# Kernel optimization log

Hardware: AMD Instinct MI355X
Metric: run time of the kernel (lower is better)

Reference implementation:

```python
import jax, jax.numpy as jnp
import numpy as np

EPS = 1.1920929e-07  # torch clamp_probs eps for float32
TEMP = 0.3           # sampler temperature T


def conv1d(x, w, b, pad):
    # x: [B, Cin, L], w: [Cout, Cin, K] -> [B, Cout, L']
    y = jax.lax.conv_general_dilated(x, w, window_strides=(1,), padding=[(pad, pad)],
                                     dimension_numbers=('NCH', 'OIH', 'NCH'))
    return y + b[None, :, None]


def setup_inputs() -> dict:
    key = jax.random.key(0)
    ks = jax.random.split(key, 20)
    B, L, V, E, F, H, K = 512, 512, 100000, 100, 100, 100, 10
    p = lambda i, shape: jax.random.normal(ks[i], shape, jnp.float32) * 0.02
    return {
        'x': jax.random.randint(ks[0], (B, L), 0, V, dtype=jnp.int32),
        'u': jax.random.uniform(ks[1], (B, K, L), dtype=jnp.float32),
        'emb': p(2, (V, E)),
        'conv1_w': p(3, (F, E, 3)), 'conv1_b': p(4, (F,)),
        'gi_w': p(5, (H, F)), 'gi_b': p(6, (H,)),
        'conv2_w': p(7, (H, F, 3)), 'conv2_b': p(8, (H,)),
        'li_w': p(9, (H, H, 3)), 'li_b': p(10, (H,)),
        'conv3_w': p(11, (F, 2 * H, 1)), 'conv3_b': p(12, (F,)),
        'conv4_w': p(13, (1, F, 1)), 'conv4_b': p(14, (1,)),
        'fc1_w': p(15, (H, E)), 'fc1_b': p(16, (H,)),
        'head_w': p(17, (1, H)), 'head_b': p(18, (1,)),
    }


def _ti_logits(e, conv1_w, conv1_b, gi_w, gi_b, conv2_w, conv2_b,
               li_w, li_b, conv3_w, conv3_b, conv4_w, conv4_b):
    relu = jax.nn.relu
    xt = jnp.swapaxes(e, 1, 2)                       # [B, E, L]
    h = relu(conv1d(xt, conv1_w, conv1_b, 1))        # [B, F, L]
    g = relu(h.mean(axis=-1) @ gi_w.T + gi_b)        # [B, H] (AdaptiveAvgPool1d(1))
    loc = relu(conv1d(relu(conv1d(h, conv2_w, conv2_b, 1)), li_w, li_b, 1))  # [B, H, L]
    gexp = jnp.broadcast_to(g[:, :, None], loc.shape)
    z = jnp.concatenate([gexp, loc], axis=1)         # [B, 2H, L]
    z = relu(conv1d(z, conv3_w, conv3_b, 0))
    return conv1d(z, conv4_w, conv4_b, 0)            # [B, 1, L]


def reference(x, u, emb, conv1_w, conv1_b, gi_w, gi_b, conv2_w, conv2_b,
              li_w, li_b, conv3_w, conv3_b, conv4_w, conv4_b,
              fc1_w, fc1_b, head_w, head_b):
    e = emb[x]                                       # [B, L, E] embedding gather
    logits = _ti_logits(e, conv1_w, conv1_b, gi_w, gi_b, conv2_w, conv2_b,
                        li_w, li_b, conv3_w, conv3_b, conv4_w, conv4_b)
    # Gumbel top-k continuous sampling (training path)
    uc = jnp.clip(u, EPS, 1.0 - EPS)
    gumbel = -jnp.log(-jnp.log(uc))                  # [B, K, L]
    noisy = (gumbel + logits) / TEMP                 # logits [B,1,L] broadcasts over K
    csamples = jax.nn.softmax(noisy, axis=-1).max(axis=1)  # [B, L]
    # distil predictor: masked mean pooling + MLP + sigmoid head
    pooled = (e * csamples[:, :, None]).mean(axis=1)  # [B, E]
    h = jax.nn.relu(pooled @ fc1_w.T + fc1_b)
    out = jax.nn.sigmoid(h @ head_w.T + head_b)       # [B, 1]
    return out, csamples
```

## Files before the change

kernel.cpp:

```cpp
#include <hip/hip_runtime.h>
#include <math.h>

#define DEV __device__ __forceinline__

typedef __attribute__((ext_vector_type(8))) short short8;
typedef __attribute__((ext_vector_type(4))) short short4v;
typedef __attribute__((ext_vector_type(4))) float f32x4;
typedef __attribute__((ext_vector_type(2))) unsigned uint2v;

#define SSTR 136
#define ROWB (16 * SSTR * 2)

DEV short f2bf(float f) {
    unsigned u = __builtin_bit_cast(unsigned, f);
    unsigned r = (u + 0x7fffu + ((u >> 16) & 1u)) >> 16;
    return (short)r;
}

#if __has_builtin(__builtin_amdgcn_cvt_pk_bf16_f32)
DEV unsigned pk2bf(float a, float b) {
    auto v = __builtin_amdgcn_cvt_pk_bf16_f32(a, b);
    return __builtin_bit_cast(unsigned, v);
}
#else
DEV unsigned pk2bf(float a, float b) {
    return ((unsigned)(unsigned short)f2bf(a)) |
           (((unsigned)(unsigned short)f2bf(b)) << 16);
}
#endif

DEV float bfu(short s) {
    unsigned u = ((unsigned)(unsigned short)s) << 16;
    return __builtin_bit_cast(float, u);
}

__global__ __launch_bounds__(256) void emb_cvt_kernel(
    const float* __restrict__ emb, short* __restrict__ embT) {
    int t = threadIdx.x;
    int row = blockIdx.x * 8 + (t >> 5);
    int c4 = t & 31;
    if (c4 >= 28) return;
    short4v v = {0, 0, 0, 0};
    if (c4 < 25) {
        f32x4 e = *(const f32x4*)&emb[row * 100 + c4 * 4];
#pragma unroll
        for (int r = 0; r < 4; ++r) v[r] = f2bf(e[r]);
    }
    *(short4v*)&embT[row * 112 + c4 * 4] = v;
}

__global__ __launch_bounds__(64) void pack_all_kernel(
    const float* __restrict__ c1w, const float* __restrict__ c2w,
    const float* __restrict__ liw, const float* __restrict__ c3w,
    short* __restrict__ A1, short* __restrict__ A2,
    short* __restrict__ A3, short* __restrict__ A4) {
    int bx = blockIdx.x;
    const float* w; short* dst; int mode, lbx;
    if (bx < 70)       { w = c1w; dst = A1; mode = 0; lbx = bx; }
    else if (bx < 140) { w = c2w; dst = A2; mode = 0; lbx = bx - 70; }
    else if (bx < 210) { w = liw; dst = A3; mode = 0; lbx = bx - 140; }
    else               { w = c3w; dst = A4; mode = 1; lbx = bx - 210; }
    int lane = threadIdx.x;
    int f = lbx % 7 * 16 + (lane & 15);
    int kb = (lbx / 7) * 32 + (lane >> 4) * 8;
    short8 v;
#pragma unroll
    for (int j = 0; j < 8; ++j) {
        int kk = kb + j;
        float val = 0.f;
        if (f < 100) {
            if (mode == 0) {
                int oct = kk >> 3, dk = oct / 13;
                int c = (oct - 13 * dk) * 8 + (kk & 7);
                if (dk < 3 && c < 100) val = w[(f * 100 + c) * 3 + dk];
            } else {
                if (kk < 100) val = w[f * 200 + 100 + kk];
            }
        }
        v[j] = f2bf(val);
    }
    *(short8*)&dst[(lbx * 64 + lane) * 8] = v;
}

template<int MT, int NT, int MTB, int NTB, bool CLAMPL, bool POOL,
         bool TO_GLOBAL, bool EDGE>
DEV void ctap(const short* __restrict__ Ap, const short* s_src, short* s_dst,
              short* __restrict__ gout, const int* bofs, const int* bofs4,
              const float* __restrict__ bias, int row0l, int l0,
              float* __restrict__ hpart_slot, int lane) {
    const int q = lane >> 4, n = lane & 15;
    const f32x4 z4 = {0.f, 0.f, 0.f, 0.f};
    f32x4 acc[MT][NT];
#pragma unroll
    for (int mt = 0; mt < MT; ++mt) {
        int fb = (MTB + mt) * 16 + q * 4;
        f32x4 bs = (fb < 100) ? *(const f32x4*)&bias[fb] : z4;
#pragma unroll
        for (int nt = 0; nt < NT; ++nt) acc[mt][nt] = bs;
    }
#pragma unroll
    for (int ks = 0; ks < 10; ++ks) {
        short8 a[MT];
#pragma unroll
        for (int mt = 0; mt < MT; ++mt)
            a[mt] = *(const short8*)&Ap[(ks * 448 + (MTB + mt) * 64 + lane) * 8];
        const char* bp = (const char*)s_src + bofs[ks];
        short8 bf[NT];
#pragma unroll
        for (int nt = 0; nt < NT; ++nt) {
            if (CLAMPL && (NTB + nt) == 4)
                bf[nt] = *(const short8*)((const char*)s_src + bofs4[ks]);
            else
                bf[nt] = *(const short8*)(bp + (NTB + nt) * ROWB);
        }
#pragma unroll
        for (int mt = 0; mt < MT; ++mt)
#pragma unroll
            for (int nt = 0; nt < NT; ++nt)
                acc[mt][nt] = __builtin_amdgcn_mfma_f32_16x16x32_bf16(
                    a[mt], bf[nt], acc[mt][nt], 0, 0, 0);
    }
    f32x4 ps[MT];
    if constexpr (POOL) {
#pragma unroll
        for (int mt = 0; mt < MT; ++mt) ps[mt] = z4;
    }
#pragma unroll
    for (int nt = 0; nt < NT; ++nt) {
        const int j = (NTB + nt) * 16 + n;
        const int l = row0l + j;
        bool lok = true;
        if constexpr (EDGE) lok = ((unsigned)l < 512u);
        const bool pok = POOL && (l >= l0) && (l < l0 + 64);
#pragma unroll
        for (int mt = 0; mt < MT; ++mt) {
            const int fb = (MTB + mt) * 16 + q * 4;
            f32x4 v;
#pragma unroll
            for (int r = 0; r < 4; ++r) {
                v[r] = fmaxf(acc[mt][nt][r], 0.f);
                if constexpr (EDGE) v[r] = lok ? v[r] : 0.f;
            }
            if constexpr (POOL) {
                if (pok) {
#pragma unroll
                    for (int r = 0; r < 4; ++r) ps[mt][r] += v[r];
                }
            }
            uint2v pk;
            pk[0] = pk2bf(v[0], v[1]); pk[1] = pk2bf(v[2], v[3]);
            if constexpr (TO_GLOBAL) {
                *(uint2v*)&gout[j * 112 + fb] = pk;
            } else {
                if ((NTB + nt) < 4 || n < 6)
                    *(uint2v*)&s_dst[j * SSTR + fb] = pk;
            }
        }
    }
    if constexpr (POOL) {
#pragma unroll
        for (int mt = 0; mt < MT; ++mt)
#pragma unroll
            for (int off = 1; off <= 8; off <<= 1)
#pragma unroll
                for (int r = 0; r < 4; ++r)
                    ps[mt][r] += __shfl_xor(ps[mt][r], off, 64);
        if (n == 0) {
#pragma unroll
            for (int mt = 0; mt < MT; ++mt)
                *(f32x4*)&hpart_slot[(MTB + mt) * 16 + q * 4] = ps[mt];
        }
    }
}

__global__ __launch_bounds__(256, 4) void fused_conv_kernel(
    const int* __restrict__ xidx, const short* __restrict__ embT,
    const short* __restrict__ A1, const short* __restrict__ A2,
    const short* __restrict__ A3,
    const float* __restrict__ b1, const float* __restrict__ b2,
    const float* __restrict__ b3,
    short* __restrict__ locT, float* __restrict__ hpart) {
    extern __shared__ char smem[];
    short* s_e = (short*)smem;
    short* s_h = (short*)(smem + 72 * SSTR * 2);
    const int tid = threadIdx.x;
    const int b = blockIdx.y, bx = blockIdx.x, l0 = bx * 64;
    const int lane = tid & 63, wv = tid >> 6;
    const int q = lane >> 4, n = lane & 15;

#pragma unroll
    for (int p = 0; p < 5; ++p) {
        int idx = tid + p * 256;
        int j = idx >> 4, c8 = idx & 15;
        if (j < 70 && c8 < 14) {
            int lg = l0 - 3 + j;
            short8 v = {0, 0, 0, 0, 0, 0, 0, 0};
            if (lg >= 0 && lg < 512) {
                int row = xidx[b * 512 + lg];
                v = *(const short8*)&embT[row * 112 + c8 * 8];
            }
            *(short8*)&s_e[j * SSTR + c8 * 8] = v;
        }
    }

    int bofs[10], bofs4[10];
#pragma unroll
    for (int ks = 0; ks < 10; ++ks) {
        int oct = ks * 4 + q;
        int dk = (oct >= 39) ? 3 : (oct >= 26) ? 2 : (oct >= 13) ? 1 : 0;
        int c0 = (oct - 13 * dk) * 8;
        bofs[ks] = ((n + dk) * SSTR + c0) * 2;
        int r4 = 64 + n + dk; if (r4 > 69) r4 = 69;
        bofs4[ks] = (r4 * SSTR + c0) * 2;
    }
    float* hps = hpart + ((b * 8 + bx) * 2 + (wv & 1)) * 112;
    short* gouts = locT + ((size_t)b * 512 + l0) * 112;

    __syncthreads();
    const bool edge = (bx == 0) || (bx == 7);

#define PASS3T(Ap, SRC, DST, BIAS, R0L, PL, E)                                   \
    if (wv == 0)      ctap<4,3,0,0,false,PL,false,E>(Ap,SRC,DST,nullptr,bofs,bofs4,BIAS,R0L,l0,hps,lane); \
    else if (wv == 1) ctap<4,2,0,3,true, PL,false,E>(Ap,SRC,DST,nullptr,bofs,bofs4,BIAS,R0L,l0,hps,lane); \
    else if (wv == 2) ctap<3,3,4,0,false,PL,false,E>(Ap,SRC,DST,nullptr,bofs,bofs4,BIAS,R0L,l0,hps,lane); \
    else              ctap<3,2,4,3,true, PL,false,E>(Ap,SRC,DST,nullptr,bofs,bofs4,BIAS,R0L,l0,hps,lane);

    if (edge) {
        PASS3T(A1, s_e, s_h, b1, l0 - 2, true, true)
        __syncthreads();
        PASS3T(A2, s_h, s_e, b2, l0 - 1, false, true)
    } else {
        PASS3T(A1, s_e, s_h, b1, l0 - 2, true, false)
        __syncthreads();
        PASS3T(A2, s_h, s_e, b2, l0 - 1, false, false)
    }
    __syncthreads();
    if (wv == 0)      ctap<4,2,0,0,false,false,true,false>(A3,s_e,nullptr,gouts,bofs,bofs4,b3,l0,l0,hps,lane);
    else if (wv == 1) ctap<4,2,0,2,false,false,true,false>(A3,s_e,nullptr,gouts,bofs,bofs4,b3,l0,l0,hps,lane);
    else if (wv == 2) ctap<3,2,4,0,false,false,true,false>(A3,s_e,nullptr,gouts,bofs,bofs4,b3,l0,l0,hps,lane);
    else              ctap<3,2,4,2,false,false,true,false>(A3,s_e,nullptr,gouts,bofs,bofs4,b3,l0,l0,hps,lane);
#undef PASS3T
}

template<int MT, int MTB, int NTB, int SLOT>
DEV void c3tile(const short* s_in, float* s_part, const short* __restrict__ A4,
                const float* __restrict__ zg, const float* __restrict__ w4,
                int bb, int lane) {
    const int q = lane >> 4, n = lane & 15;
    const f32x4 z4 = {0.f, 0.f, 0.f, 0.f};
    f32x4 acc[MT][2];
#pragma unroll
    for (int mt = 0; mt < MT; ++mt) {
        int fb = (MTB + mt) * 16 + q * 4;
        f32x4 zgv = *(const f32x4*)&zg[bb * 112 + fb];
#pragma unroll
        for (int nt = 0; nt < 2; ++nt) acc[mt][nt] = zgv;
    }
#pragma unroll
    for (int ks = 0; ks < 4; ++ks) {
        short8 a[MT];
#pragma unroll
        for (int mt = 0; mt < MT; ++mt)
            a[mt] = *(const short8*)&A4[(ks * 448 + (MTB + mt) * 64 + lane) * 8];
        int c0 = (ks * 4 + q) * 8;
        if (c0 > 104) c0 = 104;
        const char* bp = (const char*)(s_in + n * SSTR + c0);
        short8 bf[2];
#pragma unroll
        for (int nt = 0; nt < 2; ++nt)
            bf[nt] = *(const short8*)(bp + (NTB + nt) * ROWB);
#pragma unroll
        for (int mt = 0; mt < MT; ++mt)
#pragma unroll
            for (int nt = 0; nt < 2; ++nt)
                acc[mt][nt] = __builtin_amdgcn_mfma_f32_16x16x32_bf16(
                    a[mt], bf[nt], acc[mt][nt], 0, 0, 0);
    }
#pragma unroll
    for (int nt = 0; nt < 2; ++nt) {
        float part = 0.f;
#pragma unroll
        for (int mt = 0; mt < MT; ++mt) {
            const int fb = (MTB + mt) * 16 + q * 4;
            f32x4 w4v = (fb < 100) ? *(const f32x4*)&w4[fb] : z4;
#pragma unroll
            for (int r = 0; r < 4; ++r)
                part += fmaxf(acc[mt][nt][r], 0.f) * w4v[r];
        }
        part += __shfl_xor(part, 16, 64);
        part += __shfl_xor(part, 32, 64);
        if (q == 0) s_part[SLOT * 64 + (NTB + nt) * 16 + n] = part;
    }
}

__global__ __launch_bounds__(256) void conv3_logits_kernel(
    const short* __restrict__ locT, const short* __restrict__ A4,
    const float* __restrict__ zg, const float* __restrict__ w4,
    const float* __restrict__ b4, float* __restrict__ logits) {
    extern __shared__ char smem[];
    short* s_in = (short*)smem;
    float* s_part = (float*)(smem + 64 * SSTR * 2);
    const int tid = threadIdx.x;
    const int b = blockIdx.y, l0r = blockIdx.x * 64;
    const int lane = tid & 63, wv = tid >> 6;

    {
        short8 tmp[4];
#pragma unroll
        for (int p = 0; p < 4; ++p) {
            int idx = tid + p * 256;
            int j = idx >> 4, c8 = idx & 15;
            if (c8 < 14)
                tmp[p] = *(const short8*)&locT[((size_t)b * 512 + l0r + j) * 112 + c8 * 8];
        }
#pragma unroll
        for (int p = 0; p < 4; ++p) {
            int idx = tid + p * 256;
            int j = idx >> 4, c8 = idx & 15;
            if (c8 < 14)
                *(short8*)&s_in[j * SSTR + c8 * 8] = tmp[p];
        }
    }
    __syncthreads();
    if (wv == 0)      c3tile<4, 0, 0, 0>(s_in, s_part, A4, zg, w4, b, lane);
    else if (wv == 1) c3tile<4, 0, 2, 0>(s_in, s_part, A4, zg, w4, b, lane);
    else if (wv == 2) c3tile<3, 4, 0, 1>(s_in, s_part, A4, zg, w4, b, lane);
    else              c3tile<3, 4, 2, 1>(s_in, s_part, A4, zg, w4, b, lane);
    __syncthreads();
    if (tid < 64)
        logits[b * 512 + l0r + tid] = s_part[tid] + s_part[64 + tid] + b4[0];
}

__global__ __launch_bounds__(128) void pool_gate_kernel(
    const float* __restrict__ hpart, const float* __restrict__ gi_w,
    const float* __restrict__ gi_b, const float* __restrict__ w3,
    const float* __restrict__ b3, float* __restrict__ zg) {
    int b = blockIdx.x, tid = threadIdx.x;
    __shared__ float s_hm[112];
    __shared__ float s_g[100];
    if (tid < 112) {
        float a = 0.f;
#pragma unroll
        for (int s = 0; s < 16; ++s) a += hpart[(b * 16 + s) * 112 + tid];
        s_hm[tid] = a * (1.f / 512.f);
    }
    __syncthreads();
    if (tid < 100) {
        float a = gi_b[tid];
        for (int f = 0; f < 100; ++f) a += s_hm[f] * gi_w[tid * 100 + f];
        s_g[tid] = fmaxf(a, 0.f);
    }
    __syncthreads();
    if (tid < 112) {
        float a = 0.f;
        if (tid < 100) {
            a = b3[tid];
            for (int h = 0; h < 100; ++h) a += s_g[h] * w3[tid * 200 + h];
        }
        zg[b * 112 + tid] = a;
    }
}

__global__ __launch_bounds__(512) void samp_head_kernel(
    const float* __restrict__ u, const float* __restrict__ logits,
    const int* __restrict__ xidx, const short* __restrict__ embT,
    const float* __restrict__ f1w, const float* __restrict__ f1b,
    const float* __restrict__ hw, const float* __restrict__ hb,
    float* __restrict__ cs_out, float* __restrict__ out) {
    const float EPSV = 1.1920929e-07f;
    const float INVT = 1.f / 0.3f;
    int b = blockIdx.x, tid = threadIdx.x;
    int lane = tid & 63, wv = tid >> 6;
    __shared__ float s_logT[512], s_cs[512];
    __shared__ int s_x[512];
    __shared__ char s_buf[16384];
    __shared__ float s_pool[112], s_h2[100], s_fin[8];
    float* s_csw = (float*)s_buf;
    float (*s_acc)[112] = (float(*)[112])s_buf;
    if (tid < 512) {
        s_logT[tid] = logits[b * 512 + tid] * INVT;
        s_x[tid] = xidx[b * 512 + tid];
    }
    __syncthreads();
    const int nk = (wv < 2) ? 2 : 1;
    float csl[8];
#pragma unroll
    for (int i = 0; i < 8; ++i) csl[i] = 0.f;
    float lt[8];
#pragma unroll
    for (int i = 0; i < 8; ++i) lt[i] = s_logT[lane * 8 + i];
    for (int j = 0; j < nk; ++j) {
        int k = wv + 8 * j;
        f32x4 u0 = *(const f32x4*)&u[(b * 10 + k) * 512 + lane * 8];
        f32x4 u1 = *(const f32x4*)&u[(b * 10 + k) * 512 + lane * 8 + 4];
        float nz[8];
#pragma unroll
        for (int i = 0; i < 8; ++i) {
            float vv = (i < 4) ? u0[i] : u1[i - 4];
            vv = fminf(fmaxf(vv, EPSV), 1.f - EPSV);
            nz[i] = -__logf(-__logf(vv)) * INVT + lt[i];
        }
        float m = nz[0];
#pragma unroll
        for (int i = 1; i < 8; ++i) m = fmaxf(m, nz[i]);
#pragma unroll
        for (int off = 1; off <= 32; off <<= 1) m = fmaxf(m, __shfl_xor(m, off, 64));
        float e[8], s = 0.f;
#pragma unroll
        for (int i = 0; i < 8; ++i) { e[i] = __expf(nz[i] - m); s += e[i]; }
#pragma unroll
        for (int off = 1; off <= 32; off <<= 1) s += __shfl_xor(s, off, 64);
        float inv = 1.f / s;
#pragma unroll
        for (int i = 0; i < 8; ++i) csl[i] = fmaxf(csl[i], e[i] * inv);
    }
#pragma unroll
    for (int i = 0; i < 8; ++i) s_csw[wv * 512 + lane * 8 + i] = csl[i];
    __syncthreads();
    {
        float c = s_csw[tid];
#pragma unroll
        for (int w = 1; w < 8; ++w) c = fmaxf(c, s_csw[w * 512 + tid]);
        s_cs[tid] = c;
        cs_out[b * 512 + tid] = c;
    }
    __syncthreads();
    int jg = tid >> 4, c8 = tid & 15;
    f32x4 pa = {0.f, 0.f, 0.f, 0.f}, pb = {0.f, 0.f, 0.f, 0.f};
    if (c8 < 14) {
#pragma unroll 4
        for (int l = jg; l < 512; l += 32) {
            int row = s_x[l];
            float cv = s_cs[l];
            short8 e8 = *(const short8*)&embT[(size_t)row * 112 + c8 * 8];
#pragma unroll
            for (int r = 0; r < 4; ++r) {
                pa[r] += cv * bfu(e8[r]);
                pb[r] += cv * bfu(e8[4 + r]);
            }
        }
    }
    __syncthreads();
    if (c8 < 14) {
        *(f32x4*)&s_acc[jg][c8 * 8] = pa;
        *(f32x4*)&s_acc[jg][c8 * 8 + 4] = pb;
    }
    __syncthreads();
    if (tid < 112) {
        float p = 0.f;
#pragma unroll
        for (int g = 0; g < 32; ++g) p += s_acc[g][tid];
        s_pool[tid] = p * (1.f / 512.f);
    }
    __syncthreads();
    if (tid < 100) {
        float a = f1b[tid];
        for (int i = 0; i < 100; ++i) a += s_pool[i] * f1w[tid * 100 + i];
        s_h2[tid] = fmaxf(a, 0.f);
    }
    __syncthreads();
    float v = (tid < 100) ? s_h2[tid] * hw[tid] : 0.f;
#pragma unroll
    for (int off = 32; off >= 1; off >>= 1) v += __shfl_xor(v, off, 64);
    if (lane == 0) s_fin[wv] = v;
    __syncthreads();
    if (tid == 0) {
        float z = hb[0];
#pragma unroll
        for (int w = 0; w < 8; ++w) z += s_fin[w];
        out[b] = 1.f / (1.f + __expf(-z));
    }
}

extern "C" void kernel_launch(void* const* d_in, const int* in_sizes, int n_in,
                              void* d_out, int out_size, void* d_ws, size_t ws_size,
                              hipStream_t stream) {
    const int*   x   = (const int*)d_in[0];
    const float* u   = (const float*)d_in[1];
    const float* emb = (const float*)d_in[2];
    const float* c1w = (const float*)d_in[3];
    const float* c1b = (const float*)d_in[4];
    const float* giw = (const float*)d_in[5];
    const float* gib = (const float*)d_in[6];
    const float* c2w = (const float*)d_in[7];
    const float* c2b = (const float*)d_in[8];
    const float* liw = (const float*)d_in[9];
    const float* lib = (const float*)d_in[10];
    const float* c3w = (const float*)d_in[11];
    const float* c3b = (const float*)d_in[12];
    const float* c4w = (const float*)d_in[13];
    const float* c4b = (const float*)d_in[14];
    const float* f1w = (const float*)d_in[15];
    const float* f1b = (const float*)d_in[16];
    const float* hww = (const float*)d_in[17];
    const float* hbb = (const float*)d_in[18];
    float* out = (float*)d_out;

    char* ws = (char*)d_ws;
    short* locT   = (short*)(ws + 0);
    short* embT   = (short*)(ws + 58720256);
    short* A1     = (short*)(ws + 81120256);
    short* A2     = (short*)(ws + 81191936);
    short* A3     = (short*)(ws + 81263616);
    short* A4     = (short*)(ws + 81335296);
    float* zg     = (float*)(ws + 81363968);
    float* logits = (float*)(ws + 81593344);
    float* hpart  = (float*)(ws + 82641920);

    emb_cvt_kernel<<<12500, 256, 0, stream>>>(emb, embT);
    pack_all_kernel<<<238, 64, 0, stream>>>(c1w, c2w, liw, c3w, A1, A2, A3, A4);

    size_t smemA = 2 * 72 * SSTR * 2;
    fused_conv_kernel<<<dim3(8, 512), 256, smemA, stream>>>(
        x, embT, A1, A2, A3, c1b, c2b, lib, locT, hpart);
    pool_gate_kernel<<<512, 128, 0, stream>>>(hpart, giw, gib, c3w, c3b, zg);
    size_t smemB = 64 * SSTR * 2 + 2 * 64 * 4;
    conv3_logits_kernel<<<dim3(8, 512), 256, smemB, stream>>>(
        locT, A4, zg, c4w, c4b, logits);
    samp_head_kernel<<<512, 512, 0, stream>>>(
        u, logits, x, embT, f1w, f1b, hww, hbb, out + 512, out);
}
```

Measured before the change: 254.6 us.

## Move kernel split point: conv1 alone, fuse conv2/li/conv3/conv4 into one kernel

The old fused kernel ran conv1, conv2 and li with recomputed halos and wrote loc to global, and a second kernel then read it back for conv3/conv4. Now conv1 runs alone, without halo recompute, and writes h to global plus the pooled partial sums. A second kernel loads h with a 2-row halo and runs conv2, li, conv3 and conv4 in shared memory, producing logits directly. This drops the redundant halo rows in conv1 and removes the loc round trip, but conv2_logits uses more shared memory and more registers.

After: 263.2 us. +3.3%, slower.

```diff
diff --git a/kernel.cpp b/kernel.cpp
--- a/kernel.cpp
+++ b/kernel.cpp
@@ -82,11 +82,11 @@
     *(short8*)&dst[(lbx * 64 + lane) * 8] = v;
 }
 
-template<int MT, int NT, int MTB, int NTB, bool CLAMPL, bool POOL,
-         bool TO_GLOBAL, bool EDGE>
+template<int MT, int NT, int MTB, int NTB, int FULLT, int NREM,
+         bool CLAMPL, bool POOL, bool TO_GLOBAL, bool EDGE>
 DEV void ctap(const short* __restrict__ Ap, const short* s_src, short* s_dst,
               short* __restrict__ gout, const int* bofs, const int* bofs4,
-              const float* __restrict__ bias, int row0l, int l0,
+              const float* __restrict__ bias, int row0l,
               float* __restrict__ hpart_slot, int lane) {
     const int q = lane >> 4, n = lane & 15;
     const f32x4 z4 = {0.f, 0.f, 0.f, 0.f};
@@ -128,10 +128,8 @@
 #pragma unroll
     for (int nt = 0; nt < NT; ++nt) {
         const int j = (NTB + nt) * 16 + n;
-        const int l = row0l + j;
         bool lok = true;
-        if constexpr (EDGE) lok = ((unsigned)l < 512u);
-        const bool pok = POOL && (l >= l0) && (l < l0 + 64);
+        if constexpr (EDGE) lok = ((unsigned)(row0l + j) < 512u);
 #pragma unroll
         for (int mt = 0; mt < MT; ++mt) {
             const int fb = (MTB + mt) * 16 + q * 4;
@@ -142,17 +140,15 @@
                 if constexpr (EDGE) v[r] = lok ? v[r] : 0.f;
             }
             if constexpr (POOL) {
-                if (pok) {
-#pragma unroll
-                    for (int r = 0; r < 4; ++r) ps[mt][r] += v[r];
-                }
+#pragma unroll
+                for (int r = 0; r < 4; ++r) ps[mt][r] += v[r];
             }
             uint2v pk;
             pk[0] = pk2bf(v[0], v[1]); pk[1] = pk2bf(v[2], v[3]);
             if constexpr (TO_GLOBAL) {
                 *(uint2v*)&gout[j * 112 + fb] = pk;
             } else {
-                if ((NTB + nt) < 4 || n < 6)
+                if ((NTB + nt) < FULLT || n < NREM)
                     *(uint2v*)&s_dst[j * SSTR + fb] = pk;
             }
         }
@@ -173,16 +169,12 @@
     }
 }
 
-__global__ __launch_bounds__(256, 4) void fused_conv_kernel(
+__global__ __launch_bounds__(256, 6) void conv1_kernel(
     const int* __restrict__ xidx, const short* __restrict__ embT,
-    const short* __restrict__ A1, const short* __restrict__ A2,
-    const short* __restrict__ A3,
-    const float* __restrict__ b1, const float* __restrict__ b2,
-    const float* __restrict__ b3,
-    short* __restrict__ locT, float* __restrict__ hpart) {
+    const short* __restrict__ A1, const float* __restrict__ b1,
+    short* __restrict__ h, float* __restrict__ hpart) {
     extern __shared__ char smem[];
     short* s_e = (short*)smem;
-    short* s_h = (short*)(smem + 72 * SSTR * 2);
     const int tid = threadIdx.x;
     const int b = blockIdx.y, bx = blockIdx.x, l0 = bx * 64;
     const int lane = tid & 63, wv = tid >> 6;
@@ -192,8 +184,8 @@
     for (int p = 0; p < 5; ++p) {
         int idx = tid + p * 256;
         int j = idx >> 4, c8 = idx & 15;
-        if (j < 70 && c8 < 14) {
-            int lg = l0 - 3 + j;
+        if (j < 66 && c8 < 14) {
+            int lg = l0 - 1 + j;
             short8 v = {0, 0, 0, 0, 0, 0, 0, 0};
             if (lg >= 0 && lg < 512) {
                 int row = xidx[b * 512 + lg];
@@ -202,133 +194,21 @@
             *(short8*)&s_e[j * SSTR + c8 * 8] = v;
         }
     }
-
-    int bofs[10], bofs4[10];
+    int bofs[10];
 #pragma unroll
     for (int ks = 0; ks < 10; ++ks) {
         int oct = ks * 4 + q;
         int dk = (oct >= 39) ? 3 : (oct >= 26) ? 2 : (oct >= 13) ? 1 : 0;
         int c0 = (oct - 13 * dk) * 8;
         bofs[ks] = ((n + dk) * SSTR + c0) * 2;
-        int r4 = 64 + n + dk; if (r4 > 69) r4 = 69;
-        bofs4[ks] = (r4 * SSTR + c0) * 2;
     }
     float* hps = hpart + ((b * 8 + bx) * 2 + (wv & 1)) * 112;
-    short* gouts = locT + ((size_t)b * 512 + l0) * 112;
-
-    __syncthreads();
-    const bool edge = (bx == 0) || (bx == 7);
-
-#define PASS3T(Ap, SRC, DST, BIAS, R0L, PL, E)                                   \
-    if (wv == 0)      ctap<4,3,0,0,false,PL,false,E>(Ap,SRC,DST,nullptr,bofs,bofs4,BIAS,R0L,l0,hps,lane); \
-    else if (wv == 1) ctap<4,2,0,3,true, PL,false,E>(Ap,SRC,DST,nullptr,bofs,bofs4,BIAS,R0L,l0,hps,lane); \
-    else if (wv == 2) ctap<3,3,4,0,false,PL,false,E>(Ap,SRC,DST,nullptr,bofs,bofs4,BIAS,R0L,l0,hps,lane); \
-    else              ctap<3,2,4,3,true, PL,false,E>(Ap,SRC,DST,nullptr,bofs,bofs4,BIAS,R0L,l0,hps,lane);
-
-    if (edge) {
-        PASS3T(A1, s_e, s_h, b1, l0 - 2, true, true)
-        __syncthreads();
-        PASS3T(A2, s_h, s_e, b2, l0 - 1, false, true)
-    } else {
-        PASS3T(A1, s_e, s_h, b1, l0 - 2, true, false)
-        __syncthreads();
-        PASS3T(A2, s_h, s_e, b2, l0 - 1, false, false)
-    }
-    __syncthreads();
-    if (wv == 0)      ctap<4,2,0,0,false,false,true,false>(A3,s_e,nullptr,gouts,bofs,bofs4,b3,l0,l0,hps,lane);
-    else if (wv == 1) ctap<4,2,0,2,false,false,true,false>(A3,s_e,nullptr,gouts,bofs,bofs4,b3,l0,l0,hps,lane);
-    else if (wv == 2) ctap<3,2,4,0,false,false,true,false>(A3,s_e,nullptr,gouts,bofs,bofs4,b3,l0,l0,hps,lane);
-    else              ctap<3,2,4,2,false,false,true,false>(A3,s_e,nullptr,gouts,bofs,bofs4,b3,l0,l0,hps,lane);
-#undef PASS3T
-}
-
-template<int MT, int MTB, int NTB, int SLOT>
-DEV void c3tile(const short* s_in, float* s_part, const short* __restrict__ A4,
-                const float* __restrict__ zg, const float* __restrict__ w4,
-                int bb, int lane) {
-    const int q = lane >> 4, n = lane & 15;
-    const f32x4 z4 = {0.f, 0.f, 0.f, 0.f};
-    f32x4 acc[MT][2];
-#pragma unroll
-    for (int mt = 0; mt < MT; ++mt) {
-        int fb = (MTB + mt) * 16 + q * 4;
-        f32x4 zgv = *(const f32x4*)&zg[bb * 112 + fb];
-#pragma unroll
-        for (int nt = 0; nt < 2; ++nt) acc[mt][nt] = zgv;
-    }
-#pragma unroll
-    for (int ks = 0; ks < 4; ++ks) {
-        short8 a[MT];
-#pragma unroll
-        for (int mt = 0; mt < MT; ++mt)
-            a[mt] = *(const short8*)&A4[(ks * 448 + (MTB + mt) * 64 + lane) * 8];
-        int c0 = (ks * 4 + q) * 8;
-        if (c0 > 104) c0 = 104;
-        const char* bp = (const char*)(s_in + n * SSTR + c0);
-        short8 bf[2];
-#pragma unroll
-        for (int nt = 0; nt < 2; ++nt)
-            bf[nt] = *(const short8*)(bp + (NTB + nt) * ROWB);
-#pragma unroll
-        for (int mt = 0; mt < MT; ++mt)
-#pragma unroll
-            for (int nt = 0; nt < 2; ++nt)
-                acc[mt][nt] = __builtin_amdgcn_mfma_f32_16x16x32_bf16(
-                    a[mt], bf[nt], acc[mt][nt], 0, 0, 0);
-    }
-#pragma unroll
-    for (int nt = 0; nt < 2; ++nt) {
-        float part = 0.f;
-#pragma unroll
-        for (int mt = 0; mt < MT; ++mt) {
-            const int fb = (MTB + mt) * 16 + q * 4;
-            f32x4 w4v = (fb < 100) ? *(const f32x4*)&w4[fb] : z4;
-#pragma unroll
-            for (int r = 0; r < 4; ++r)
-                part += fmaxf(acc[mt][nt][r], 0.f) * w4v[r];
-        }
-        part += __shfl_xor(part, 16, 64);
-        part += __shfl_xor(part, 32, 64);
-        if (q == 0) s_part[SLOT * 64 + (NTB + nt) * 16 + n] = part;
-    }
-}
-
-__global__ __launch_bounds__(256) void conv3_logits_kernel(
-    const short* __restrict__ locT, const short* __restrict__ A4,
-    const float* __restrict__ zg, const float* __restrict__ w4,
-    const float* __restrict__ b4, float* __restrict__ logits) {
-    extern __shared__ char smem[];
-    short* s_in = (short*)smem;
-    float* s_part = (float*)(smem + 64 * SSTR * 2);
-    const int tid = threadIdx.x;
-    const int b = blockIdx.y, l0r = blockIdx.x * 64;
-    const int lane = tid & 63, wv = tid >> 6;
-
-    {
-        short8 tmp[4];
-#pragma unroll
-        for (int p = 0; p < 4; ++p) {
-            int idx = tid + p * 256;
-            int j = idx >> 4, c8 = idx & 15;
-            if (c8 < 14)
-                tmp[p] = *(const short8*)&locT[((size_t)b * 512 + l0r + j) * 112 + c8 * 8];
-        }
-#pragma unroll
-        for (int p = 0; p < 4; ++p) {
-            int idx = tid + p * 256;
-            int j = idx >> 4, c8 = idx & 15;
-            if (c8 < 14)
-                *(short8*)&s_in[j * SSTR + c8 * 8] = tmp[p];
-        }
-    }
-    __syncthreads();
-    if (wv == 0)      c3tile<4, 0, 0, 0>(s_in, s_part, A4, zg, w4, b, lane);
-    else if (wv == 1) c3tile<4, 0, 2, 0>(s_in, s_part, A4, zg, w4, b, lane);
-    else if (wv == 2) c3tile<3, 4, 0, 1>(s_in, s_part, A4, zg, w4, b, lane);
-    else              c3tile<3, 4, 2, 1>(s_in, s_part, A4, zg, w4, b, lane);
-    __syncthreads();
-    if (tid < 64)
-        logits[b * 512 + l0r + tid] = s_part[tid] + s_part[64 + tid] + b4[0];
+    short* gouts = h + ((size_t)b * 512 + l0) * 112;
+    __syncthreads();
+    if (wv == 0)      ctap<4,2,0,0,8,0,false,true,true,false>(A1,s_e,nullptr,gouts,bofs,nullptr,b1,l0,hps,lane);
+    else if (wv == 1) ctap<4,2,0,2,8,0,false,true,true,false>(A1,s_e,nullptr,gouts,bofs,nullptr,b1,l0,hps,lane);
+    else if (wv == 2) ctap<3,2,4,0,8,0,false,true,true,false>(A1,s_e,nullptr,gouts,bofs,nullptr,b1,l0,hps,lane);
+    else              ctap<3,2,4,2,8,0,false,true,true,false>(A1,s_e,nullptr,gouts,bofs,nullptr,b1,l0,hps,lane);
 }
 
 __global__ __launch_bounds__(128) void pool_gate_kernel(
@@ -359,6 +239,122 @@
         }
         zg[b * 112 + tid] = a;
     }
+}
+
+template<int MT, int MTB, int NTB, int SLOT>
+DEV void c3tile(const short* s_in, float* s_part, const short* __restrict__ A4,
+                const float* __restrict__ zg, const float* __restrict__ w4,
+                int bb, int lane) {
+    const int q = lane >> 4, n = lane & 15;
+    const f32x4 z4 = {0.f, 0.f, 0.f, 0.f};
+    f32x4 acc[MT][2];
+#pragma unroll
+    for (int mt = 0; mt < MT; ++mt) {
+        int fb = (MTB + mt) * 16 + q * 4;
+        f32x4 zgv = *(const f32x4*)&zg[bb * 112 + fb];
+#pragma unroll
+        for (int nt = 0; nt < 2; ++nt) acc[mt][nt] = zgv;
+    }
+#pragma unroll
+    for (int ks = 0; ks < 4; ++ks) {
+        short8 a[MT];
+#pragma unroll
+        for (int mt = 0; mt < MT; ++mt)
+            a[mt] = *(const short8*)&A4[(ks * 448 + (MTB + mt) * 64 + lane) * 8];
+        int c0 = (ks * 4 + q) * 8;
+        if (c0 > 104) c0 = 104;
+        const char* bp = (const char*)(s_in + n * SSTR + c0);
+        short8 bf[2];
+#pragma unroll
+        for (int nt = 0; nt < 2; ++nt)
+            bf[nt] = *(const short8*)(bp + (NTB + nt) * ROWB);
+#pragma unroll
+        for (int mt = 0; mt < MT; ++mt)
+#pragma unroll
+            for (int nt = 0; nt < 2; ++nt)
+                acc[mt][nt] = __builtin_amdgcn_mfma_f32_16x16x32_bf16(
+                    a[mt], bf[nt], acc[mt][nt], 0, 0, 0);
+    }
+#pragma unroll
+    for (int nt = 0; nt < 2; ++nt) {
+        float part = 0.f;
+#pragma unroll
+        for (int mt = 0; mt < MT; ++mt) {
+            const int fb = (MTB + mt) * 16 + q * 4;
+            f32x4 w4v = (fb < 100) ? *(const f32x4*)&w4[fb] : z4;
+#pragma unroll
+            for (int r = 0; r < 4; ++r)
+                part += fmaxf(acc[mt][nt][r], 0.f) * w4v[r];
+        }
+        part += __shfl_xor(part, 16, 64);
+        part += __shfl_xor(part, 32, 64);
+        if (q == 0) s_part[SLOT * 64 + (NTB + nt) * 16 + n] = part;
+    }
+}
+
+__global__ __launch_bounds__(256, 4) void conv2_logits_kernel(
+    const short* __restrict__ h, const short* __restrict__ A2,
+    const short* __restrict__ A3, const short* __restrict__ A4,
+    const float* __restrict__ b2, const float* __restrict__ b3,
+    const float* __restrict__ zg, const float* __restrict__ w4,
+    const float* __restrict__ b4, float* __restrict__ logits) {
+    extern __shared__ char smem[];
+    short* bufA = (short*)smem;
+    short* bufB = (short*)(smem + 68 * SSTR * 2);
+    float* s_part = (float*)(smem + (68 + 66) * SSTR * 2);
+    const int tid = threadIdx.x;
+    const int b = blockIdx.y, bx = blockIdx.x, l0 = bx * 64;
+    const int lane = tid & 63, wv = tid >> 6;
+    const int q = lane >> 4, n = lane & 15;
+
+#pragma unroll
+    for (int p = 0; p < 5; ++p) {
+        int idx = tid + p * 256;
+        int j = idx >> 4, c8 = idx & 15;
+        if (j < 68 && c8 < 14) {
+            int lg = l0 - 2 + j;
+            short8 v = {0, 0, 0, 0, 0, 0, 0, 0};
+            if (lg >= 0 && lg < 512)
+                v = *(const short8*)&h[((size_t)b * 512 + lg) * 112 + c8 * 8];
+            *(short8*)&bufA[j * SSTR + c8 * 8] = v;
+        }
+    }
+    int bofs[10], bofs4[10];
+#pragma unroll
+    for (int ks = 0; ks < 10; ++ks) {
+        int oct = ks * 4 + q;
+        int dk = (oct >= 39) ? 3 : (oct >= 26) ? 2 : (oct >= 13) ? 1 : 0;
+        int c0 = (oct - 13 * dk) * 8;
+        bofs[ks] = ((n + dk) * SSTR + c0) * 2;
+        int r4 = 64 + n + dk; if (r4 > 67) r4 = 67;
+        bofs4[ks] = (r4 * SSTR + c0) * 2;
+    }
+    __syncthreads();
+    const bool edge = (bx == 0) || (bx == 7);
+    if (edge) {
+        if (wv == 0)      ctap<4,3,0,0,4,2,false,false,false,true>(A2,bufA,bufB,nullptr,bofs,bofs4,b2,l0-1,nullptr,lane);
+        else if (wv == 1) ctap<4,2,0,3,4,2,true, false,false,true>(A2,bufA,bufB,nullptr,bofs,bofs4,b2,l0-1,nullptr,lane);
+        else if (wv == 2) ctap<3,3,4,0,4,2,false,false,false,true>(A2,bufA,bufB,nullptr,bofs,bofs4,b2,l0-1,nullptr,lane);
+        else              ctap<3,2,4,3,4,2,true, false,false,true>(A2,bufA,bufB,nullptr,bofs,bofs4,b2,l0-1,nullptr,lane);
+    } else {
+        if (wv == 0)      ctap<4,3,0,0,4,2,false,false,false,false>(A2,bufA,bufB,nullptr,bofs,bofs4,b2,l0-1,nullptr,lane);
+        else if (wv == 1) ctap<4,2,0,3,4,2,true, false,false,false>(A2,bufA,bufB,nullptr,bofs,bofs4,b2,l0-1,nullptr,lane);
+        else if (wv == 2) ctap<3,3,4,0,4,2,false,false,false,false>(A2,bufA,bufB,nullptr,bofs,bofs4,b2,l0-1,nullptr,lane);
+        else              ctap<3,2,4,3,4,2,true, false,false,false>(A2,bufA,bufB,nullptr,bofs,bofs4,b2,l0-1,nullptr,lane);
+    }
+    __syncthreads();
+    if (wv == 0)      ctap<4,2,0,0,8,0,false,false,false,false>(A3,bufB,bufA,nullptr,bofs,nullptr,b3,l0,nullptr,lane);
+    else if (wv == 1) ctap<4,2,0,2,8,0,false,false,false,false>(A3,bufB,bufA,nullptr,bofs,nullptr,b3,l0,nullptr,lane);
+    else if (wv == 2) ctap<3,2,4,0,8,0,false,false,false,false>(A3,bufB,bufA,nullptr,bofs,nullptr,b3,l0,nullptr,lane);
+    else              ctap<3,2,4,2,8,0,false,false,false,false>(A3,bufB,bufA,nullptr,bofs,nullptr,b3,l0,nullptr,lane);
+    __syncthreads();
+    if (wv == 0)      c3tile<4, 0, 0, 0>(bufA, s_part, A4, zg, w4, b, lane);
+    else if (wv == 1) c3tile<4, 0, 2, 0>(bufA, s_part, A4, zg, w4, b, lane);
+    else if (wv == 2) c3tile<3, 4, 0, 1>(bufA, s_part, A4, zg, w4, b, lane);
+    else              c3tile<3, 4, 2, 1>(bufA, s_part, A4, zg, w4, b, lane);
+    __syncthreads();
+    if (tid < 64)
+        logits[b * 512 + l0 + tid] = s_part[tid] + s_part[64 + tid] + b4[0];
 }
 
 __global__ __launch_bounds__(512) void samp_head_kernel(
@@ -497,7 +493,7 @@
     float* out = (float*)d_out;
 
     char* ws = (char*)d_ws;
-    short* locT   = (short*)(ws + 0);
+    short* hbuf   = (short*)(ws + 0);
     short* embT   = (short*)(ws + 58720256);
     short* A1     = (short*)(ws + 81120256);
     short* A2     = (short*)(ws + 81191936);
@@ -510,13 +506,13 @@
     emb_cvt_kernel<<<12500, 256, 0, stream>>>(emb, embT);
     pack_all_kernel<<<238, 64, 0, stream>>>(c1w, c2w, liw, c3w, A1, A2, A3, A4);
 
-    size_t smemA = 2 * 72 * SSTR * 2;
-    fused_conv_kernel<<<dim3(8, 512), 256, smemA, stream>>>(
-        x, embT, A1, A2, A3, c1b, c2b, lib, locT, hpart);
+    size_t smemA = 66 * SSTR * 2;
+    conv1_kernel<<<dim3(8, 512), 256, smemA, stream>>>(
+        x, embT, A1, c1b, hbuf, hpart);
     pool_gate_kernel<<<512, 128, 0, stream>>>(hpart, giw, gib, c3w, c3b, zg);
-    size_t smemB = 64 * SSTR * 2 + 2 * 64 * 4;
-    conv3_logits_kernel<<<dim3(8, 512), 256, smemB, stream>>>(
-        locT, A4, zg, c4w, c4b, logits);
+    size_t smemB = (68 + 66) * SSTR * 2 + 2 * 64 * 4;
+    conv2_logits_kernel<<<dim3(8, 512), 256, smemB, stream>>>(
+        hbuf, A2, A3, A4, c2b, lib, zg, c4w, c4b, logits);
     samp_head_kernel<<<512, 512, 0, stream>>>(
         u, logits, x, embT, f1w, f1b, hww, hbb, out + 512, out);
 }
```

## Merge prep kernels and split sampler/head into parallel gather stages

Applied to the files above, without the earlier changes.

Merges the embedding conversion and weight packing into one prep launch. Splits the fused sampler+head kernel into a sampler kernel (256 threads, 4 waves covering the 10 noise rows), a head_part kernel that spreads the embedding-gather pooling over 8 sequence chunks per batch (4096 blocks), and a small head_fin kernel that reduces the partials and runs the MLP. The goal is more parallelism for the memory-bound gather, which used to run with only 512 blocks. In exchange it adds two launches and a round trip of the partial sums through global memory.

After: 260.7 us. 1.02x slower.

```diff
diff --git a/kernel.cpp b/kernel.cpp
--- a/kernel.cpp
+++ b/kernel.cpp
@@ -34,33 +34,34 @@
     return __builtin_bit_cast(float, u);
 }
 
-__global__ __launch_bounds__(256) void emb_cvt_kernel(
-    const float* __restrict__ emb, short* __restrict__ embT) {
-    int t = threadIdx.x;
-    int row = blockIdx.x * 8 + (t >> 5);
-    int c4 = t & 31;
-    if (c4 >= 28) return;
-    short4v v = {0, 0, 0, 0};
-    if (c4 < 25) {
-        f32x4 e = *(const f32x4*)&emb[row * 100 + c4 * 4];
-#pragma unroll
-        for (int r = 0; r < 4; ++r) v[r] = f2bf(e[r]);
-    }
-    *(short4v*)&embT[row * 112 + c4 * 4] = v;
-}
-
-__global__ __launch_bounds__(64) void pack_all_kernel(
+__global__ __launch_bounds__(256) void prep_kernel(
+    const float* __restrict__ emb, short* __restrict__ embT,
     const float* __restrict__ c1w, const float* __restrict__ c2w,
     const float* __restrict__ liw, const float* __restrict__ c3w,
     short* __restrict__ A1, short* __restrict__ A2,
     short* __restrict__ A3, short* __restrict__ A4) {
-    int bx = blockIdx.x;
+    int bxg = blockIdx.x, t = threadIdx.x;
+    if (bxg < 12500) {
+        int row = bxg * 8 + (t >> 5);
+        int c4 = t & 31;
+        if (c4 >= 28) return;
+        short4v v = {0, 0, 0, 0};
+        if (c4 < 25) {
+            f32x4 e = *(const f32x4*)&emb[row * 100 + c4 * 4];
+#pragma unroll
+            for (int r = 0; r < 4; ++r) v[r] = f2bf(e[r]);
+        }
+        *(short4v*)&embT[row * 112 + c4 * 4] = v;
+        return;
+    }
+    int bx = (bxg - 12500) * 4 + (t >> 6);
+    if (bx >= 238) return;
+    int lane = t & 63;
     const float* w; short* dst; int mode, lbx;
     if (bx < 70)       { w = c1w; dst = A1; mode = 0; lbx = bx; }
     else if (bx < 140) { w = c2w; dst = A2; mode = 0; lbx = bx - 70; }
     else if (bx < 210) { w = liw; dst = A3; mode = 0; lbx = bx - 140; }
     else               { w = c3w; dst = A4; mode = 1; lbx = bx - 210; }
-    int lane = threadIdx.x;
     int f = lbx % 7 * 16 + (lane & 15);
     int kb = (lbx / 7) * 32 + (lane >> 4) * 8;
     short8 v;
@@ -361,28 +362,19 @@
     }
 }
 
-__global__ __launch_bounds__(512) void samp_head_kernel(
+__global__ __launch_bounds__(256) void sampler_kernel(
     const float* __restrict__ u, const float* __restrict__ logits,
-    const int* __restrict__ xidx, const short* __restrict__ embT,
-    const float* __restrict__ f1w, const float* __restrict__ f1b,
-    const float* __restrict__ hw, const float* __restrict__ hb,
-    float* __restrict__ cs_out, float* __restrict__ out) {
+    float* __restrict__ cs_out) {
     const float EPSV = 1.1920929e-07f;
     const float INVT = 1.f / 0.3f;
     int b = blockIdx.x, tid = threadIdx.x;
     int lane = tid & 63, wv = tid >> 6;
-    __shared__ float s_logT[512], s_cs[512];
-    __shared__ int s_x[512];
-    __shared__ char s_buf[16384];
-    __shared__ float s_pool[112], s_h2[100], s_fin[8];
-    float* s_csw = (float*)s_buf;
-    float (*s_acc)[112] = (float(*)[112])s_buf;
-    if (tid < 512) {
-        s_logT[tid] = logits[b * 512 + tid] * INVT;
-        s_x[tid] = xidx[b * 512 + tid];
-    }
-    __syncthreads();
-    const int nk = (wv < 2) ? 2 : 1;
+    __shared__ float s_logT[512];
+    __shared__ float s_csw[4][512];
+    for (int l = tid; l < 512; l += 256)
+        s_logT[l] = logits[b * 512 + l] * INVT;
+    __syncthreads();
+    const int nk = (wv < 2) ? 3 : 2;
     float csl[8];
 #pragma unroll
     for (int i = 0; i < 8; ++i) csl[i] = 0.f;
@@ -390,7 +382,7 @@
 #pragma unroll
     for (int i = 0; i < 8; ++i) lt[i] = s_logT[lane * 8 + i];
     for (int j = 0; j < nk; ++j) {
-        int k = wv + 8 * j;
+        int k = wv + 4 * j;
         f32x4 u0 = *(const f32x4*)&u[(b * 10 + k) * 512 + lane * 8];
         f32x4 u1 = *(const f32x4*)&u[(b * 10 + k) * 512 + lane * 8 + 4];
         float nz[8];
@@ -415,23 +407,35 @@
         for (int i = 0; i < 8; ++i) csl[i] = fmaxf(csl[i], e[i] * inv);
     }
 #pragma unroll
-    for (int i = 0; i < 8; ++i) s_csw[wv * 512 + lane * 8 + i] = csl[i];
-    __syncthreads();
-    {
-        float c = s_csw[tid];
-#pragma unroll
-        for (int w = 1; w < 8; ++w) c = fmaxf(c, s_csw[w * 512 + tid]);
-        s_cs[tid] = c;
-        cs_out[b * 512 + tid] = c;
+    for (int i = 0; i < 8; ++i) s_csw[wv][lane * 8 + i] = csl[i];
+    __syncthreads();
+    for (int l = tid; l < 512; l += 256)
+        cs_out[b * 512 + l] = fmaxf(fmaxf(s_csw[0][l], s_csw[1][l]),
+                                    fmaxf(s_csw[2][l], s_csw[3][l]));
+}
+
+__global__ __launch_bounds__(256) void head_part_kernel(
+    const int* __restrict__ xidx, const short* __restrict__ embT,
+    const float* __restrict__ cs, float* __restrict__ hp) {
+    int sb = blockIdx.x, b = blockIdx.y;
+    int tid = threadIdx.x;
+    __shared__ int s_x[64];
+    __shared__ float s_c[64];
+    __shared__ float s_acc[16][112];
+    if (tid < 64) {
+        int l = sb * 64 + tid;
+        s_x[tid] = xidx[b * 512 + l];
+        s_c[tid] = cs[b * 512 + l];
     }
     __syncthreads();
     int jg = tid >> 4, c8 = tid & 15;
-    f32x4 pa = {0.f, 0.f, 0.f, 0.f}, pb = {0.f, 0.f, 0.f, 0.f};
     if (c8 < 14) {
-#pragma unroll 4
-        for (int l = jg; l < 512; l += 32) {
+        f32x4 pa = {0.f, 0.f, 0.f, 0.f}, pb = {0.f, 0.f, 0.f, 0.f};
+#pragma unroll
+        for (int i = 0; i < 4; ++i) {
+            int l = jg + i * 16;
             int row = s_x[l];
-            float cv = s_cs[l];
+            float cv = s_c[l];
             short8 e8 = *(const short8*)&embT[(size_t)row * 112 + c8 * 8];
 #pragma unroll
             for (int r = 0; r < 4; ++r) {
@@ -439,35 +443,47 @@
                 pb[r] += cv * bfu(e8[4 + r]);
             }
         }
-    }
-    __syncthreads();
-    if (c8 < 14) {
         *(f32x4*)&s_acc[jg][c8 * 8] = pa;
         *(f32x4*)&s_acc[jg][c8 * 8 + 4] = pb;
     }
     __syncthreads();
     if (tid < 112) {
-        float p = 0.f;
-#pragma unroll
-        for (int g = 0; g < 32; ++g) p += s_acc[g][tid];
-        s_pool[tid] = p * (1.f / 512.f);
+        float v = 0.f;
+#pragma unroll
+        for (int g = 0; g < 16; ++g) v += s_acc[g][tid];
+        hp[(b * 8 + sb) * 112 + tid] = v;
+    }
+}
+
+__global__ __launch_bounds__(128) void head_fin_kernel(
+    const float* __restrict__ hp, const float* __restrict__ fc1_w,
+    const float* __restrict__ fc1_b, const float* __restrict__ head_w,
+    const float* __restrict__ head_b, float* __restrict__ out) {
+    int b = blockIdx.x, tid = threadIdx.x;
+    int lane = tid & 63, wv = tid >> 6;
+    __shared__ float s_pool[112];
+    __shared__ float s_h2[100];
+    __shared__ float s_red[2];
+    if (tid < 112) {
+        float a = 0.f;
+#pragma unroll
+        for (int sb = 0; sb < 8; ++sb) a += hp[(b * 8 + sb) * 112 + tid];
+        s_pool[tid] = a * (1.f / 512.f);
     }
     __syncthreads();
     if (tid < 100) {
-        float a = f1b[tid];
-        for (int i = 0; i < 100; ++i) a += s_pool[i] * f1w[tid * 100 + i];
-        s_h2[tid] = fmaxf(a, 0.f);
-    }
-    __syncthreads();
-    float v = (tid < 100) ? s_h2[tid] * hw[tid] : 0.f;
+        float acc = fc1_b[tid];
+        for (int i = 0; i < 100; ++i) acc += s_pool[i] * fc1_w[tid * 100 + i];
+        s_h2[tid] = fmaxf(acc, 0.f);
+    }
+    __syncthreads();
+    float v = (tid < 100) ? s_h2[tid] * head_w[tid] : 0.f;
 #pragma unroll
     for (int off = 32; off >= 1; off >>= 1) v += __shfl_xor(v, off, 64);
-    if (lane == 0) s_fin[wv] = v;
+    if (lane == 0) s_red[wv] = v;
     __syncthreads();
     if (tid == 0) {
-        float z = hb[0];
-#pragma unroll
-        for (int w = 0; w < 8; ++w) z += s_fin[w];
+        float z = s_red[0] + s_red[1] + head_b[0];
         out[b] = 1.f / (1.f + __expf(-z));
     }
 }
@@ -506,9 +522,10 @@
     float* zg     = (float*)(ws + 81363968);
     float* logits = (float*)(ws + 81593344);
     float* hpart  = (float*)(ws + 82641920);
-
-    emb_cvt_kernel<<<12500, 256, 0, stream>>>(emb, embT);
-    pack_all_kernel<<<238, 64, 0, stream>>>(c1w, c2w, liw, c3w, A1, A2, A3, A4);
+    float* hp     = (float*)(ws + 86311936);
+
+    prep_kernel<<<12560, 256, 0, stream>>>(
+        emb, embT, c1w, c2w, liw, c3w, A1, A2, A3, A4);
 
     size_t smemA = 2 * 72 * SSTR * 2;
     fused_conv_kernel<<<dim3(8, 512), 256, smemA, stream>>>(
@@ -517,6 +534,7 @@
     size_t smemB = 64 * SSTR * 2 + 2 * 64 * 4;
     conv3_logits_kernel<<<dim3(8, 512), 256, smemB, stream>>>(
         locT, A4, zg, c4w, c4b, logits);
-    samp_head_kernel<<<512, 512, 0, stream>>>(
-        u, logits, x, embT, f1w, f1b, hww, hbb, out + 512, out);
-}
+    sampler_kernel<<<512, 256, 0, stream>>>(u, logits, out + 512);
+    head_part_kernel<<<dim3(8, 512), 256, 0, stream>>>(x, embT, out + 512, hp);
+    head_fin_kernel<<<512, 128, 0, stream>>>(hp, f1w, f1b, hww, hbb, out);
+}
```
